# Kernel tuning notes

Hardware: AMD Instinct MI355X
Metric: run time of the kernel (lower is better)

Reference implementation:

```python
import jax, jax.numpy as jnp
import numpy as np

IN_FEATURES = 8192
OUT_FEATURES = 14336
M_TOKENS = 64


def _dequant_rowwise_int4(w_packed, w_scales):
    # w_packed: [out, in//2], each byte holds two signed int4 values
    # (low nibble = even k index, high nibble = odd k index, two's complement)
    low = w_packed & 0xF
    high = (w_packed >> 4) & 0xF
    q = jnp.stack([low, high], axis=-1).reshape(w_packed.shape[0], -1)  # [out, in]
    q = jnp.where(q >= 8, q - 16, q).astype(jnp.float32)
    return q * w_scales[:, None]  # [out, in]


def setup_inputs() -> dict:
    key = jax.random.key(0)
    k1, k2, k3, k4 = jax.random.split(key, 4)
    x = jax.random.normal(k1, (M_TOKENS, IN_FEATURES), dtype=jnp.float32)
    w_packed = jax.random.randint(k2, (OUT_FEATURES, IN_FEATURES // 2), 0, 256, dtype=jnp.int32)
    # per-row scales, small positive values as produced by max-abs/7 quantization
    w_scales = jax.random.uniform(k3, (OUT_FEATURES,), dtype=jnp.float32) * 0.02 + 1e-4
    bias = jax.random.normal(k4, (OUT_FEATURES,), dtype=jnp.float32)
    return {"x": x, "w_packed": w_packed, "w_scales": w_scales, "bias": bias}


def reference(x, w_packed, w_scales, bias):
    original_shape = x.shape[:-1]
    x_2d = x.reshape(-1, IN_FEATURES)
    w = _dequant_rowwise_int4(w_packed, w_scales)  # [out, in]
    y = x_2d @ w.T + bias[None, :]  # [M, out]
    return y.reshape(*original_shape, OUT_FEATURES)
```

## Files before the change

kernel.cpp:

```cpp
#include <hip/hip_runtime.h>

#define IN_F   8192
#define OUT_F  14336
#define M_TOK  64
#define KPI    4096
#define NBLK   448
#define KSPLIT 4
#define PSTR   (M_TOK * OUT_F)

typedef __attribute__((ext_vector_type(8))) short          bf16x8;
typedef __attribute__((ext_vector_type(8))) unsigned short u16x8;
typedef __attribute__((ext_vector_type(4))) float          f32x4;

__device__ __forceinline__ unsigned short f2bf_rne(float f) {
    unsigned u = __builtin_bit_cast(unsigned, f);
    u += 0x7FFFu + ((u >> 16) & 1u);
    return (unsigned short)(u >> 16);
}

__global__ __launch_bounds__(256) void qlin_prep(const float* __restrict__ x,
                                                 unsigned short* __restrict__ xs) {
    int tid  = blockIdx.x * 256 + threadIdx.x;
    int lane = tid & 63;
    int mt   = (tid >> 6) & 3;
    int fg   = tid >> 8;
    int q = lane >> 4, t = lane & 15;
    const float* src = x + (size_t)(mt * 16 + t) * IN_F + fg * 32 + q * 8;
    u16x8 o;
#pragma unroll
    for (int j = 0; j < 8; ++j) o[j] = f2bf_rne(src[j]);
    *reinterpret_cast<u16x8*>(xs + (size_t)tid * 8) = o;
}

__global__ __launch_bounds__(256) void qlin_repack(const int* __restrict__ wp,
                                                   unsigned* __restrict__ rep) {
    __shared__ unsigned lds[2048];
    const int G   = blockIdx.x >> 3;
    const int g8  = blockIdx.x & 7;
    const int tid = threadIdx.x;
    const int r = tid >> 4, T = tid & 15;
    const int q = T & 3, i = T >> 2;
    const int* src = wp + (size_t)(G * 16 + r) * KPI + T * 4;
#pragma unroll
    for (int j = 0; j < 8; ++j) {
        const int g = g8 * 8 + j;
        int4 v = *reinterpret_cast<const int4*>(src + 64 * g);
        unsigned d = (unsigned)(v.x & 255) | ((unsigned)(v.y & 255) << 8)
                   | ((unsigned)(v.z & 255) << 16) | ((unsigned)(v.w & 255) << 24);
        lds[j * 256 + q * 64 + r * 4 + i] = d;
    }
    __syncthreads();
    unsigned* dst = rep + ((size_t)G * 64 + g8 * 8) * 256;
#pragma unroll
    for (int s = 0; s < 2; ++s)
        *reinterpret_cast<uint4*>(dst + s * 1024 + tid * 4) =
            *reinterpret_cast<const uint4*>(&lds[s * 1024 + tid * 4]);
}

__device__ __forceinline__ int unpack2_bf16(int v) {
    int q0 = ((int)((unsigned)v << 28)) >> 28;
    int q1 = ((int)((unsigned)v << 24)) >> 28;
    unsigned u0 = __builtin_bit_cast(unsigned, (float)q0);
    unsigned u1 = __builtin_bit_cast(unsigned, (float)q1);
    return (int)((u0 >> 16) | (u1 & 0xFFFF0000u));
}

__device__ __forceinline__ bf16x8 unpack_frag(unsigned d) {
    int4 pk;
    pk.x = unpack2_bf16((int)(d));
    pk.y = unpack2_bf16((int)(d >> 8));
    pk.z = unpack2_bf16((int)(d >> 16));
    pk.w = unpack2_bf16((int)(d >> 24));
    return __builtin_bit_cast(bf16x8, pk);
}

__global__ __launch_bounds__(256, 4) void qlin_gemm(const unsigned short* __restrict__ xs,
                                                    const unsigned* __restrict__ rep,
                                                    float* __restrict__ part) {
    __shared__ float red[4 * 2048];
    const int tid  = threadIdx.x;
    const int wave = tid >> 6;
    const int lane = tid & 63;
    const int t = lane & 15;
    const int q = lane >> 4;

    const int nb   = blockIdx.x % NBLK;
    const int kblk = blockIdx.x / NBLK;
    const int g0   = kblk * 16 + wave * 4;

    const unsigned* b0p = rep + ((size_t)((nb * 2)     * 64 + g0) * 64 + q * 16 + t) * 4;
    const unsigned* b1p = rep + ((size_t)((nb * 2 + 1) * 64 + g0) * 64 + q * 16 + t) * 4;

    f32x4 acc[2][4] = {};

#pragma unroll
    for (int gi = 0; gi < 4; ++gi) {
        uint4 w0 = *reinterpret_cast<const uint4*>(b0p + (size_t)gi * 256);
        uint4 w1 = *reinterpret_cast<const uint4*>(b1p + (size_t)gi * 256);
        const unsigned* d0 = reinterpret_cast<const unsigned*>(&w0);
        const unsigned* d1 = reinterpret_cast<const unsigned*>(&w1);
#pragma unroll
        for (int i = 0; i < 4; ++i) {
            bf16x8 b0 = unpack_frag(d0[i]);
            bf16x8 b1 = unpack_frag(d1[i]);
            const int F = (g0 + gi) * 4 + i;
#pragma unroll
            for (int mt = 0; mt < 4; ++mt) {
                bf16x8 a = *reinterpret_cast<const bf16x8*>(
                    xs + ((size_t)(F * 4 + mt) * 64 + lane) * 8);
                acc[0][mt] = __builtin_amdgcn_mfma_f32_16x16x32_bf16(a, b0, acc[0][mt], 0, 0, 0);
                acc[1][mt] = __builtin_amdgcn_mfma_f32_16x16x32_bf16(a, b1, acc[1][mt], 0, 0, 0);
            }
        }
    }

#pragma unroll
    for (int ng = 0; ng < 2; ++ng)
#pragma unroll
        for (int mt = 0; mt < 4; ++mt)
#pragma unroll
            for (int r = 0; r < 4; ++r)
                red[wave * 2048 + (mt * 16 + q * 4 + r) * 32 + ng * 16 + t] = acc[ng][mt][r];
    __syncthreads();

    const int m  = tid >> 2;
    const int nq = tid & 3;
    float* p = part + (size_t)kblk * PSTR + (size_t)m * OUT_F + nb * 32 + nq * 8;
    float4 v0, v1;
#pragma unroll
    for (int e = 0; e < 4; ++e) {
        const int a0 = m * 32 + nq * 8 + e;
        const int a1 = a0 + 4;
        v0[e] = red[a0] + red[2048 + a0] + red[4096 + a0] + red[6144 + a0];
        v1[e] = red[a1] + red[2048 + a1] + red[4096 + a1] + red[6144 + a1];
    }
    *reinterpret_cast<float4*>(p)     = v0;
    *reinterpret_cast<float4*>(p + 4) = v1;
}

__global__ __launch_bounds__(256) void qlin_reduce(const float* __restrict__ part,
                                                   const float* __restrict__ scales,
                                                   const float* __restrict__ bias,
                                                   float* __restrict__ out) {
    int g  = blockIdx.x * 256 + threadIdx.x;
    int n4 = g % (OUT_F / 4);
    float4 s4 = reinterpret_cast<const float4*>(scales)[n4];
    float4 b4 = reinterpret_cast<const float4*>(bias)[n4];
    float4 a = {0.f, 0.f, 0.f, 0.f};
#pragma unroll
    for (int s = 0; s < KSPLIT; ++s) {
        float4 v = reinterpret_cast<const float4*>(part)[(size_t)s * (PSTR / 4) + g];
        a.x += v.x; a.y += v.y; a.z += v.z; a.w += v.w;
    }
    float4 o;
    o.x = a.x * s4.x + b4.x;
    o.y = a.y * s4.y + b4.y;
    o.z = a.z * s4.z + b4.z;
    o.w = a.w * s4.w + b4.w;
    reinterpret_cast<float4*>(out)[g] = o;
}

extern "C" void kernel_launch(void* const* d_in, const int* in_sizes, int n_in,
                              void* d_out, int out_size, void* d_ws, size_t ws_size,
                              hipStream_t stream) {
    const float* x    = (const float*)d_in[0];
    const int*   wp   = (const int*)d_in[1];
    const float* sc   = (const float*)d_in[2];
    const float* bias = (const float*)d_in[3];
    float* out = (float*)d_out;

    unsigned short* xs   = (unsigned short*)d_ws;
    unsigned*       rp   = (unsigned*)((char*)d_ws + (1 << 20));
    float*          part = (float*)((char*)d_ws + (64u << 20));

    qlin_prep<<<256, 256, 0, stream>>>(x, xs);
    qlin_repack<<<896 * 8, 256, 0, stream>>>(wp, rp);
    qlin_gemm<<<NBLK * KSPLIT, 256, 0, stream>>>(xs, rp, part);
    qlin_reduce<<<(M_TOK * OUT_F) / 4 / 256, 256, 0, stream>>>(part, sc, bias, out);
}
```

Measured before the change: 370.7 us.

## Widen GEMM block N tile to 128 columns to reuse activation fragments

Each GEMM block now covers 128 output columns (8 groups of 16) instead of 32, and loads the activation fragments once per k-subgroup into registers, reusing them across the 8 weight groups. This cuts redundant activation loads and reduces the block count. In exchange it raises register pressure (32 accumulator tiles), drops occupancy to 2 blocks per CU, doubles LDS use, and splits the cross-wave reduction into two halves with an extra barrier. Fewer blocks (448) may also reduce latency hiding on the weight stream.

```diff
diff --git a/kernel.cpp b/kernel.cpp
--- a/kernel.cpp
+++ b/kernel.cpp
@@ -4,7 +4,7 @@
 #define OUT_F  14336
 #define M_TOK  64
 #define KPI    4096
-#define NBLK   448
+#define NBLK   112
 #define KSPLIT 4
 #define PSTR   (M_TOK * OUT_F)
 
@@ -74,10 +74,10 @@
     return __builtin_bit_cast(bf16x8, pk);
 }
 
-__global__ __launch_bounds__(256, 4) void qlin_gemm(const unsigned short* __restrict__ xs,
+__global__ __launch_bounds__(256, 2) void qlin_gemm(const unsigned short* __restrict__ xs,
                                                     const unsigned* __restrict__ rep,
                                                     float* __restrict__ part) {
-    __shared__ float red[4 * 2048];
+    __shared__ float red[4 * 128 * 32];
     const int tid  = threadIdx.x;
     const int wave = tid >> 6;
     const int lane = tid & 63;
@@ -88,54 +88,66 @@
     const int kblk = blockIdx.x / NBLK;
     const int g0   = kblk * 16 + wave * 4;
 
-    const unsigned* b0p = rep + ((size_t)((nb * 2)     * 64 + g0) * 64 + q * 16 + t) * 4;
-    const unsigned* b1p = rep + ((size_t)((nb * 2 + 1) * 64 + g0) * 64 + q * 16 + t) * 4;
+    const unsigned* wbase = rep + ((size_t)(nb * 8 * 64 + g0) * 64 + lane) * 4;
 
-    f32x4 acc[2][4] = {};
+    f32x4 acc[8][4] = {};
 
 #pragma unroll
-    for (int gi = 0; gi < 4; ++gi) {
-        uint4 w0 = *reinterpret_cast<const uint4*>(b0p + (size_t)gi * 256);
-        uint4 w1 = *reinterpret_cast<const uint4*>(b1p + (size_t)gi * 256);
-        const unsigned* d0 = reinterpret_cast<const unsigned*>(&w0);
-        const unsigned* d1 = reinterpret_cast<const unsigned*>(&w1);
+    for (int sub = 0; sub < 4; ++sub) {
+        const int g = g0 + sub;
+        bf16x8 a[4][4];
 #pragma unroll
-        for (int i = 0; i < 4; ++i) {
-            bf16x8 b0 = unpack_frag(d0[i]);
-            bf16x8 b1 = unpack_frag(d1[i]);
-            const int F = (g0 + gi) * 4 + i;
+        for (int i = 0; i < 4; ++i)
 #pragma unroll
-            for (int mt = 0; mt < 4; ++mt) {
-                bf16x8 a = *reinterpret_cast<const bf16x8*>(
-                    xs + ((size_t)(F * 4 + mt) * 64 + lane) * 8);
-                acc[0][mt] = __builtin_amdgcn_mfma_f32_16x16x32_bf16(a, b0, acc[0][mt], 0, 0, 0);
-                acc[1][mt] = __builtin_amdgcn_mfma_f32_16x16x32_bf16(a, b1, acc[1][mt], 0, 0, 0);
+            for (int mt = 0; mt < 4; ++mt)
+                a[i][mt] = *reinterpret_cast<const bf16x8*>(
+                    xs + ((size_t)((g * 4 + i) * 4 + mt) * 64 + lane) * 8);
+#pragma unroll
+        for (int ng = 0; ng < 8; ++ng) {
+            uint4 wd = *reinterpret_cast<const uint4*>(
+                wbase + (size_t)ng * 16384 + sub * 256);
+            const unsigned* d = reinterpret_cast<const unsigned*>(&wd);
+#pragma unroll
+            for (int i = 0; i < 4; ++i) {
+                bf16x8 b = unpack_frag(d[i]);
+#pragma unroll
+                for (int mt = 0; mt < 4; ++mt)
+                    acc[ng][mt] = __builtin_amdgcn_mfma_f32_16x16x32_bf16(
+                        a[i][mt], b, acc[ng][mt], 0, 0, 0);
             }
         }
     }
 
 #pragma unroll
-    for (int ng = 0; ng < 2; ++ng)
+    for (int h = 0; h < 2; ++h) {
+        if (h) __syncthreads();
 #pragma unroll
-        for (int mt = 0; mt < 4; ++mt)
+        for (int ng = 0; ng < 8; ++ng)
 #pragma unroll
-            for (int r = 0; r < 4; ++r)
-                red[wave * 2048 + (mt * 16 + q * 4 + r) * 32 + ng * 16 + t] = acc[ng][mt][r];
-    __syncthreads();
+            for (int mi = 0; mi < 2; ++mi)
+#pragma unroll
+                for (int r = 0; r < 4; ++r)
+                    red[wave * 4096 + (ng * 16 + t) * 32 + mi * 16 + q * 4 + r] =
+                        acc[ng][h * 2 + mi][r];
+        __syncthreads();
 
-    const int m  = tid >> 2;
-    const int nq = tid & 3;
-    float* p = part + (size_t)kblk * PSTR + (size_t)m * OUT_F + nb * 32 + nq * 8;
-    float4 v0, v1;
+        const int ml = tid >> 3;
+        const int nq = tid & 7;
+        float* p = part + (size_t)kblk * PSTR
+                 + (size_t)(h * 32 + ml) * OUT_F + nb * 128;
 #pragma unroll
-    for (int e = 0; e < 4; ++e) {
-        const int a0 = m * 32 + nq * 8 + e;
-        const int a1 = a0 + 4;
-        v0[e] = red[a0] + red[2048 + a0] + red[4096 + a0] + red[6144 + a0];
-        v1[e] = red[a1] + red[2048 + a1] + red[4096 + a1] + red[6144 + a1];
+        for (int j = 0; j < 4; ++j) {
+            const int nf = nq + j * 8;
+            float4 v;
+#pragma unroll
+            for (int e = 0; e < 4; ++e) {
+                const int nl = nf * 4 + e;
+                v[e] = red[0 * 4096 + nl * 32 + ml] + red[1 * 4096 + nl * 32 + ml]
+                     + red[2 * 4096 + nl * 32 + ml] + red[3 * 4096 + nl * 32 + ml];
+            }
+            *reinterpret_cast<float4*>(p + nf * 4) = v;
+        }
     }
-    *reinterpret_cast<float4*>(p)     = v0;
-    *reinterpret_cast<float4*>(p + 4) = v1;
 }
 
 __global__ __launch_bounds__(256) void qlin_reduce(const float* __restrict__ part,
```

New measurement: 368.3 us. About the same (-0.6%).
